# Performance work log

Measured on AMD Instinct MI355X. Metric: run time of the kernel, lower is better.

## Reference

```python
import jax, jax.numpy as jnp
import numpy as np

HIDDEN = 1024
HEADS = 16
HEAD_SIZE = HIDDEN // HEADS


def setup_inputs() -> dict:
    key = jax.random.key(0)
    k0, k1, k2, k3 = jax.random.split(key, 4)
    scale = 1.0 / np.sqrt(HIDDEN)
    return {
        "input_data": jax.random.normal(k0, (4, 4096, HIDDEN), dtype=jnp.float32),
        "W0": jax.random.normal(k1, (HIDDEN, HIDDEN), dtype=jnp.float32) * scale,
        "W1": jax.random.normal(k2, (HIDDEN, HIDDEN), dtype=jnp.float32) * scale,
        "W2": jax.random.normal(k3, (HIDDEN, HIDDEN), dtype=jnp.float32) * scale,
    }


def reference(input_data, W0, W1, W2):
    b, s, _ = input_data.shape
    k, h = HEADS, HEAD_SIZE
    # torch.nn.Linear(bias=False): y = x @ W.T
    out = input_data @ W0.T          # [b, s, hidden]
    out1 = input_data @ W1.T
    out2 = input_data @ W2.T
    # reshape to heads; cummax over the sequence axis (axis=1 here, which
    # matches cummax(dim=2) on the permuted (b,k,s,h) layout in torch)
    out_h = out.reshape(b, s, k, h)
    out1_h = out1.reshape(b, s, k, h)
    cm = jax.lax.associative_scan(jnp.maximum, (out_h + out1_h) / jnp.sqrt(jnp.float32(h)), axis=1)
    cm = cm.reshape(b, s, k * h)
    out = (cm + out2) * cm + out1
    return out
```

## Files before the change

### kernel.cpp

```cpp
#include <hip/hip_runtime.h>
#include <cstdint>
#include <cstddef>

#define HIDDEN 1024
#define BATCH 4
#define SEQ 4096
#define M_ROWS (BATCH * SEQ)
#define K_DIM 1024
#define SUBCHUNK 32
#define NSUB (SEQ / SUBCHUNK)

typedef __bf16 bf16_t;
typedef __bf16 v8bf __attribute__((ext_vector_type(8)));
typedef float v4f __attribute__((ext_vector_type(4)));
typedef unsigned short us8 __attribute__((ext_vector_type(8)));

__device__ __forceinline__ unsigned short f32_to_bf16(float f) {
  unsigned int u = __float_as_uint(f);
  u += 0x7fffu + ((u >> 16) & 1u);
  return (unsigned short)(u >> 16);
}
__device__ __forceinline__ float bf16_to_f32(unsigned short u) {
  return __uint_as_float((unsigned int)u << 16);
}

__global__ void convert_kernel(const float* __restrict__ X,
                               const float* __restrict__ W0,
                               const float* __restrict__ W1,
                               const float* __restrict__ W2,
                               unsigned short* __restrict__ Xb,
                               unsigned short* __restrict__ Wb) {
  int bx = blockIdx.x;
  if (bx < 16384) {
    int i = bx * 256 + threadIdx.x;
    float4 f = ((const float4*)X)[i];
    ushort4 u;
    u.x = f32_to_bf16(f.x); u.y = f32_to_bf16(f.y);
    u.z = f32_to_bf16(f.z); u.w = f32_to_bf16(f.w);
    ((ushort4*)Xb)[i] = u;
  } else {
    int i = (bx - 16384) * 256 + threadIdx.x;
    int mat = i >> 18;
    int off = i & 0x3FFFF;
    float4 f;
    if (mat == 0) {
      float4 a = ((const float4*)W0)[off];
      float4 b = ((const float4*)W1)[off];
      f.x = (a.x + b.x) * 0.125f; f.y = (a.y + b.y) * 0.125f;
      f.z = (a.z + b.z) * 0.125f; f.w = (a.w + b.w) * 0.125f;
    } else {
      const float* src = (mat == 1) ? W1 : W2;
      f = ((const float4*)src)[off];
    }
    ushort4 u;
    u.x = f32_to_bf16(f.x); u.y = f32_to_bf16(f.y);
    u.z = f32_to_bf16(f.z); u.w = f32_to_bf16(f.w);
    ((ushort4*)Wb)[i] = u;
  }
}

__global__ __launch_bounds__(512, 2) void gemm256_kernel(
    const bf16_t* __restrict__ A, const bf16_t* __restrict__ B,
    unsigned short* __restrict__ Lp, unsigned short* __restrict__ C1p,
    unsigned short* __restrict__ C2p, float* __restrict__ cmax) {
  extern __shared__ __align__(16) char smem[];

  const int tid = threadIdx.x;
  const int wave = tid >> 6;
  const int lane = tid & 63;
  const int quad = lane >> 4;
  const int r16 = lane & 15;
  const int wr = wave >> 2;
  const int wc = wave & 3;

  const int orig = (int)blockIdx.x;
  const int swz = (orig & 7) * 96 + (orig >> 3);
  const int bx = swz % 12;
  const int mt = swz / 12;
  const int mtile0 = mt * 256;
  const int nbase = bx * 256;

  const int l3 = lane >> 3;
  const int lc = lane & 7;
  const size_t laneOff = (size_t)l3 * K_DIM + (size_t)((lc ^ l3) << 3);
  const bf16_t* Ag = A + (size_t)(mtile0 + wave * 8) * K_DIM + laneOff;
  const bf16_t* Bg = B + (size_t)(nbase + wave * 8) * K_DIM + laneOff;

  const int aRow = (wr * 128 + r16) * 128;
  const int bRow = (wc * 64 + r16) * 128;
  const int cxor = (r16 & 7) * 16;
  const int qx = quad * 16;

  v4f acc[8][4];
#pragma unroll
  for (int i = 0; i < 8; ++i)
#pragma unroll
    for (int j = 0; j < 4; ++j) acc[i][j] = (v4f)(0.0f);

  v8bf afr[4];
  v8bf bfr[4][2];

#define STG_A(d, q, kt) __builtin_amdgcn_global_load_lds( \
    (__attribute__((address_space(1))) void*)(Ag + (size_t)(q) * (64 * K_DIM) + (size_t)(kt) * 64), \
    (__attribute__((address_space(3))) void*)(smem + (d) * 32768 + (q) * 8192 + wave * 1024), 16, 0, 0)
#define STG_B(d, q, kt) __builtin_amdgcn_global_load_lds( \
    (__attribute__((address_space(1))) void*)(Bg + (size_t)(q) * (64 * K_DIM) + (size_t)(kt) * 64), \
    (__attribute__((address_space(3))) void*)(smem + 65536 + (d) * 32768 + (q) * 8192 + wave * 1024), 16, 0, 0)
#define LDA(d, i, kk) (*(const v8bf*)(smem + (d) * 32768 + aRow + (i) * 2048 + (((kk) * 64 + qx) ^ cxor)))
#define LDB(d, j, kk) (*(const v8bf*)(smem + 65536 + (d) * 32768 + bRow + (j) * 2048 + (((kk) * 64 + qx) ^ cxor)))
#define RD_A(d, ih, kk) { _Pragma("unroll") for (int ii = 0; ii < 4; ++ii) afr[ii] = LDA(d, (ih) * 4 + ii, kk); }
#define RD_B(d, kk) { _Pragma("unroll") for (int j = 0; j < 4; ++j) bfr[j][kk] = LDB(d, j, kk); }
#define MM(ih, kk) \
  __builtin_amdgcn_s_barrier(); \
  asm volatile("s_waitcnt lgkmcnt(0)" ::: "memory"); \
  __builtin_amdgcn_s_setprio(1); \
  { _Pragma("unroll") for (int ii = 0; ii < 4; ++ii) { _Pragma("unroll") for (int j = 0; j < 4; ++j) \
      acc[(ih) * 4 + ii][j] = __builtin_amdgcn_mfma_f32_16x16x32_bf16(afr[ii], bfr[j][(kk)], acc[(ih) * 4 + ii][j], 0, 0, 0); } } \
  __builtin_amdgcn_s_setprio(0);
#define BAR() __builtin_amdgcn_s_barrier()
#define WAITV(n) asm volatile("s_waitcnt vmcnt(" #n ")" ::: "memory")

  STG_A(0, 0, 0); STG_A(0, 1, 0); STG_A(0, 2, 0); STG_A(0, 3, 0);
  STG_B(0, 0, 0); STG_B(0, 1, 0); STG_B(0, 2, 0); STG_B(0, 3, 0);
  STG_A(1, 0, 1); STG_A(1, 2, 1); STG_B(1, 0, 1); STG_B(1, 1, 1);
  WAITV(4);
  BAR();

  for (int it = 0; it < 7; ++it) {
    const int t1 = 2 * it + 1, t2 = t1 + 1, t3 = t1 + 2;
    RD_A(0, 0, 0); RD_B(0, 0);
    STG_B(1, 2, t1); STG_B(1, 3, t1);
    MM(0, 0); BAR();
    RD_B(0, 1); RD_A(0, 0, 1);
    STG_A(1, 1, t1); STG_A(1, 3, t1);
    MM(0, 1); BAR();
    RD_A(0, 1, 0);
    STG_A(0, 0, t2); STG_A(0, 2, t2);
    MM(1, 0); BAR();
    RD_A(0, 1, 1);
    STG_B(0, 0, t2); STG_B(0, 1, t2);
    MM(1, 1); WAITV(4); BAR();
    RD_A(1, 0, 0); RD_B(1, 0);
    STG_B(0, 2, t2); STG_B(0, 3, t2);
    MM(0, 0); BAR();
    RD_B(1, 1); RD_A(1, 0, 1);
    STG_A(0, 1, t2); STG_A(0, 3, t2);
    MM(0, 1); BAR();
    RD_A(1, 1, 0);
    STG_A(1, 0, t3); STG_A(1, 2, t3);
    MM(1, 0); BAR();
    RD_A(1, 1, 1);
    STG_B(1, 0, t3); STG_B(1, 1, t3);
    MM(1, 1); WAITV(4); BAR();
  }
  RD_A(0, 0, 0); RD_B(0, 0);
  STG_B(1, 2, 15); STG_B(1, 3, 15);
  MM(0, 0); BAR();
  RD_B(0, 1); RD_A(0, 0, 1);
  STG_A(1, 1, 15); STG_A(1, 3, 15);
  MM(0, 1); BAR();
  RD_A(0, 1, 0); MM(1, 0); BAR();
  RD_A(0, 1, 1); MM(1, 1); WAITV(0); BAR();
  RD_A(1, 0, 0); RD_B(1, 0); MM(0, 0); BAR();
  RD_B(1, 1); RD_A(1, 0, 1); MM(0, 1); BAR();
  RD_A(1, 1, 0); MM(1, 0); BAR();
  RD_A(1, 1, 1); MM(1, 1);

#undef STG_A
#undef STG_B
#undef LDA
#undef LDB
#undef RD_A
#undef RD_B
#undef MM
#undef BAR
#undef WAITV

  const int mat = bx >> 2;
  const int ncol0 = (bx & 3) * 256;

  if (mat != 0) {
    unsigned short* Cm = (mat == 1) ? C1p : C2p;
#pragma unroll
    for (int i = 0; i < 8; ++i)
#pragma unroll
      for (int j = 0; j < 4; ++j)
#pragma unroll
        for (int r = 0; r < 4; ++r) {
          int row = mtile0 + wr * 128 + i * 16 + quad * 4 + r;
          int col = ncol0 + wc * 64 + j * 16 + r16;
          Cm[(size_t)row * HIDDEN + col] = f32_to_bf16(acc[i][j][r]);
        }
    return;
  }

  const int bidx = mtile0 >> 12;
  const int sub0 = (mtile0 & 4095) >> 5;
#pragma unroll
  for (int s = 0; s < 4; ++s) {
#pragma unroll
    for (int j = 0; j < 4; ++j) {
      float c0[4], c1[4];
      c0[0] = acc[s * 2][j][0];
      c1[0] = acc[s * 2 + 1][j][0];
#pragma unroll
      for (int r = 1; r < 4; ++r) {
        c0[r] = fmaxf(c0[r - 1], acc[s * 2][j][r]);
        c1[r] = fmaxf(c1[r - 1], acc[s * 2 + 1][j][r]);
      }
      float t0 = c0[3], t1 = c1[3], u;
      u = __shfl_up(t0, 16); if (quad >= 1) t0 = fmaxf(t0, u);
      u = __shfl_up(t0, 32); if (quad >= 2) t0 = fmaxf(t0, u);
      u = __shfl_up(t1, 16); if (quad >= 1) t1 = fmaxf(t1, u);
      u = __shfl_up(t1, 32); if (quad >= 2) t1 = fmaxf(t1, u);
      float e0 = __shfl_up(t0, 16); if (quad == 0) e0 = -INFINITY;
      float e1 = __shfl_up(t1, 16); if (quad == 0) e1 = -INFINITY;
      float T0 = __shfl(t0, 48 + r16);
      float T1 = __shfl(t1, 48 + r16);
      int col = ncol0 + wc * 64 + j * 16 + r16;
      int rowb = mtile0 + wr * 128 + s * 32 + quad * 4;
#pragma unroll
      for (int r = 0; r < 4; ++r) {
        float L0 = fmaxf(c0[r], e0);
        float L1 = fmaxf(fmaxf(c1[r], e1), T0);
        Lp[(size_t)(rowb + r) * HIDDEN + col] = f32_to_bf16(L0);
        Lp[(size_t)(rowb + 16 + r) * HIDDEN + col] = f32_to_bf16(L1);
      }
      if (quad == 0) {
        int sub = sub0 + wr * 4 + s;
        cmax[((size_t)bidx * NSUB + sub) * HIDDEN + col] = fmaxf(T0, T1);
      }
    }
  }
}

__global__ void prefix_kernel(const float* __restrict__ cmax,
                              float* __restrict__ pmax) {
  int col = blockIdx.x * 256 + threadIdx.x;
  int b = blockIdx.y;
  const float* cp = cmax + (size_t)b * NSUB * HIDDEN + col;
  float* pp = pmax + (size_t)b * NSUB * HIDDEN + col;
  float run = -INFINITY;
#pragma unroll 1
  for (int s0 = 0; s0 < NSUB; s0 += 16) {
    float v[16];
#pragma unroll
    for (int i = 0; i < 16; ++i) v[i] = cp[(size_t)(s0 + i) * HIDDEN];
#pragma unroll
    for (int i = 0; i < 16; ++i) {
      pp[(size_t)(s0 + i) * HIDDEN] = run;
      run = fmaxf(run, v[i]);
    }
  }
}

__global__ void final_kernel(const unsigned short* __restrict__ L,
                             const unsigned short* __restrict__ C1,
                             const unsigned short* __restrict__ C2,
                             const float* __restrict__ pmax,
                             float* __restrict__ out) {
  const int t = threadIdx.x;
  const int half = t >> 7;
  const int col = (t & 127) * 8;
  const int s = blockIdx.x * 2 + half;
  const int b = blockIdx.y;
  const int sub = s >> 5;
  const float* pv = pmax + ((size_t)b * NSUB + sub) * HIDDEN + col;
  float4 p0 = *(const float4*)pv;
  float4 p1 = *(const float4*)(pv + 4);
  float pr[8] = {p0.x, p0.y, p0.z, p0.w, p1.x, p1.y, p1.z, p1.w};
  size_t base = ((size_t)b * SEQ + s) * HIDDEN + col;
  us8 ul = *(const us8*)(L + base);
  us8 u1 = *(const us8*)(C1 + base);
  us8 u2 = *(const us8*)(C2 + base);
  float o[8];
#pragma unroll
  for (int k = 0; k < 8; ++k) {
    float m = fmaxf(pr[k], bf16_to_f32((unsigned short)ul[k]));
    o[k] = (m + bf16_to_f32((unsigned short)u2[k])) * m
           + bf16_to_f32((unsigned short)u1[k]);
  }
  float4 o0 = {o[0], o[1], o[2], o[3]};
  float4 o1 = {o[4], o[5], o[6], o[7]};
  *(float4*)(out + base) = o0;
  *(float4*)(out + base + 4) = o1;
}

extern "C" void kernel_launch(void* const* d_in, const int* in_sizes, int n_in,
                              void* d_out, int out_size, void* d_ws, size_t ws_size,
                              hipStream_t stream) {
  const float* X = (const float*)d_in[0];
  const float* W0 = (const float*)d_in[1];
  const float* W1 = (const float*)d_in[2];
  const float* W2 = (const float*)d_in[3];
  float* out = (float*)d_out;

  char* ws = (char*)d_ws;
  unsigned short* Xb = (unsigned short*)ws;
  unsigned short* Wb = (unsigned short*)(ws + 33554432);
  unsigned short* Lp = (unsigned short*)(ws + 33554432 + 6291456);
  unsigned short* C1p = (unsigned short*)(ws + 2 * 33554432 + 6291456);
  unsigned short* C2p = (unsigned short*)(ws + 3 * 33554432 + 6291456);
  float* cmax = (float*)(ws + 4 * 33554432 + 6291456);
  float* pmax = (float*)(ws + 4 * 33554432 + 6291456 + 2097152);

  convert_kernel<<<19456, 256, 0, stream>>>(X, W0, W1, W2, Xb, Wb);

  gemm256_kernel<<<768, 512, 131072, stream>>>((const bf16_t*)Xb, (const bf16_t*)Wb,
                                               Lp, C1p, C2p, cmax);

  dim3 pgrid(4, BATCH);
  prefix_kernel<<<pgrid, 256, 0, stream>>>(cmax, pmax);

  dim3 fgrid(SEQ / 2, BATCH);
  final_kernel<<<fgrid, 256, 0, stream>>>(Lp, C1p, C2p, pmax, out);
}
```

Before: 158.9 us.

## Split GEMM into scan GEMM and fused W1/W2 GEMM with epilogue

The first GEMM now computes only the (W0+W1)/8 projection, producing the bf16 logits and per-chunk maxima. A second GEMM computes the W1 and W2 projections together, sharing the A tile in LDS, and applies the prefix-max combine and final formula in its epilogue, writing fp32 output directly. This drops the bf16 C1/C2 intermediate round trip through HBM and the separate elementwise final kernel. In exchange it adds a second launch that re-stages X, uses a narrower 128-column N tile per matrix, and does uncoalesced scalar Lp/pmax reads in the epilogue.

```diff
diff --git a/kernel.cpp b/kernel.cpp
--- a/kernel.cpp
+++ b/kernel.cpp
@@ -59,10 +59,9 @@
   }
 }
 
-__global__ __launch_bounds__(512, 2) void gemm256_kernel(
+__global__ __launch_bounds__(512, 2) void gemm_s_kernel(
     const bf16_t* __restrict__ A, const bf16_t* __restrict__ B,
-    unsigned short* __restrict__ Lp, unsigned short* __restrict__ C1p,
-    unsigned short* __restrict__ C2p, float* __restrict__ cmax) {
+    unsigned short* __restrict__ Lp, float* __restrict__ cmax) {
   extern __shared__ __align__(16) char smem[];
 
   const int tid = threadIdx.x;
@@ -74,9 +73,9 @@
   const int wc = wave & 3;
 
   const int orig = (int)blockIdx.x;
-  const int swz = (orig & 7) * 96 + (orig >> 3);
-  const int bx = swz % 12;
-  const int mt = swz / 12;
+  const int swz = (orig & 7) * 32 + (orig >> 3);
+  const int bx = swz & 3;
+  const int mt = swz >> 2;
   const int mtile0 = mt * 256;
   const int nbase = bx * 256;
 
@@ -176,24 +175,7 @@
 #undef BAR
 #undef WAITV
 
-  const int mat = bx >> 2;
-  const int ncol0 = (bx & 3) * 256;
-
-  if (mat != 0) {
-    unsigned short* Cm = (mat == 1) ? C1p : C2p;
-#pragma unroll
-    for (int i = 0; i < 8; ++i)
-#pragma unroll
-      for (int j = 0; j < 4; ++j)
-#pragma unroll
-        for (int r = 0; r < 4; ++r) {
-          int row = mtile0 + wr * 128 + i * 16 + quad * 4 + r;
-          int col = ncol0 + wc * 64 + j * 16 + r16;
-          Cm[(size_t)row * HIDDEN + col] = f32_to_bf16(acc[i][j][r]);
-        }
-    return;
-  }
-
+  const int ncol0 = bx * 256;
   const int bidx = mtile0 >> 12;
   const int sub0 = (mtile0 & 4095) >> 5;
 #pragma unroll
@@ -254,36 +236,149 @@
   }
 }
 
-__global__ void final_kernel(const unsigned short* __restrict__ L,
-                             const unsigned short* __restrict__ C1,
-                             const unsigned short* __restrict__ C2,
-                             const float* __restrict__ pmax,
-                             float* __restrict__ out) {
-  const int t = threadIdx.x;
-  const int half = t >> 7;
-  const int col = (t & 127) * 8;
-  const int s = blockIdx.x * 2 + half;
-  const int b = blockIdx.y;
-  const int sub = s >> 5;
-  const float* pv = pmax + ((size_t)b * NSUB + sub) * HIDDEN + col;
-  float4 p0 = *(const float4*)pv;
-  float4 p1 = *(const float4*)(pv + 4);
-  float pr[8] = {p0.x, p0.y, p0.z, p0.w, p1.x, p1.y, p1.z, p1.w};
-  size_t base = ((size_t)b * SEQ + s) * HIDDEN + col;
-  us8 ul = *(const us8*)(L + base);
-  us8 u1 = *(const us8*)(C1 + base);
-  us8 u2 = *(const us8*)(C2 + base);
-  float o[8];
-#pragma unroll
-  for (int k = 0; k < 8; ++k) {
-    float m = fmaxf(pr[k], bf16_to_f32((unsigned short)ul[k]));
-    o[k] = (m + bf16_to_f32((unsigned short)u2[k])) * m
-           + bf16_to_f32((unsigned short)u1[k]);
-  }
-  float4 o0 = {o[0], o[1], o[2], o[3]};
-  float4 o1 = {o[4], o[5], o[6], o[7]};
-  *(float4*)(out + base) = o0;
-  *(float4*)(out + base + 4) = o1;
+__global__ __launch_bounds__(512, 2) void gemm_f_kernel(
+    const bf16_t* __restrict__ A, const bf16_t* __restrict__ B,
+    const unsigned short* __restrict__ Lp, const float* __restrict__ pmax,
+    float* __restrict__ out) {
+  extern __shared__ __align__(16) char smem[];
+
+  const int tid = threadIdx.x;
+  const int wave = tid >> 6;
+  const int lane = tid & 63;
+  const int quad = lane >> 4;
+  const int r16 = lane & 15;
+  const int wr = wave >> 2;
+  const int wc = wave & 3;
+
+  const int orig = (int)blockIdx.x;
+  const int swz = (orig & 7) * 64 + (orig >> 3);
+  const int mt = swz >> 3;
+  const int nt = swz & 7;
+  const int mtile0 = mt * 256;
+  const int ncol0 = nt * 128;
+
+  const int l3 = lane >> 3;
+  const int lc = lane & 7;
+  const size_t laneOff = (size_t)l3 * K_DIM + (size_t)((lc ^ l3) << 3);
+  const bf16_t* Ag = A + (size_t)(mtile0 + wave * 8) * K_DIM + laneOff;
+  const bf16_t* Bg1 = B + (size_t)(1024 + ncol0 + wave * 8) * K_DIM + laneOff;
+  const bf16_t* Bg2 = B + (size_t)(2048 + ncol0 + wave * 8) * K_DIM + laneOff;
+
+  const int aRow = (wr * 128 + r16) * 128;
+  const int bRow = (wc * 32 + r16) * 128;
+  const int cxor = (r16 & 7) * 16;
+  const int qx = quad * 16;
+
+  v4f acc1[8][2], acc2[8][2];
+#pragma unroll
+  for (int i = 0; i < 8; ++i)
+#pragma unroll
+    for (int j = 0; j < 2; ++j) { acc1[i][j] = (v4f)(0.0f); acc2[i][j] = (v4f)(0.0f); }
+
+  v8bf afr[4];
+  v8bf b1fr[2][2], b2fr[2][2];
+
+#define STG2_A(d, q, kt) __builtin_amdgcn_global_load_lds( \
+    (__attribute__((address_space(1))) void*)(Ag + (size_t)(q) * (64 * K_DIM) + (size_t)(kt) * 64), \
+    (__attribute__((address_space(3))) void*)(smem + (d) * 32768 + (q) * 8192 + wave * 1024), 16, 0, 0)
+#define STG2_B1(d, q, kt) __builtin_amdgcn_global_load_lds( \
+    (__attribute__((address_space(1))) void*)(Bg1 + (size_t)(q) * (64 * K_DIM) + (size_t)(kt) * 64), \
+    (__attribute__((address_space(3))) void*)(smem + 65536 + (d) * 32768 + (q) * 8192 + wave * 1024), 16, 0, 0)
+#define STG2_B2(d, q, kt) __builtin_amdgcn_global_load_lds( \
+    (__attribute__((address_space(1))) void*)(Bg2 + (size_t)(q) * (64 * K_DIM) + (size_t)(kt) * 64), \
+    (__attribute__((address_space(3))) void*)(smem + 65536 + (d) * 32768 + 16384 + (q) * 8192 + wave * 1024), 16, 0, 0)
+#define LDA2(d, i, kk) (*(const v8bf*)(smem + (d) * 32768 + aRow + (i) * 2048 + (((kk) * 64 + qx) ^ cxor)))
+#define LDB21(d, j, kk) (*(const v8bf*)(smem + 65536 + (d) * 32768 + bRow + (j) * 2048 + (((kk) * 64 + qx) ^ cxor)))
+#define LDB22(d, j, kk) (*(const v8bf*)(smem + 65536 + (d) * 32768 + 16384 + bRow + (j) * 2048 + (((kk) * 64 + qx) ^ cxor)))
+#define RD2_A(d, ih, kk) { _Pragma("unroll") for (int ii = 0; ii < 4; ++ii) afr[ii] = LDA2(d, (ih) * 4 + ii, kk); }
+#define RD2_B(d, kk) { _Pragma("unroll") for (int j = 0; j < 2; ++j) { b1fr[j][kk] = LDB21(d, j, kk); b2fr[j][kk] = LDB22(d, j, kk); } }
+#define MM2(ih, kk) \
+  __builtin_amdgcn_s_barrier(); \
+  asm volatile("s_waitcnt lgkmcnt(0)" ::: "memory"); \
+  __builtin_amdgcn_s_setprio(1); \
+  { _Pragma("unroll") for (int ii = 0; ii < 4; ++ii) { _Pragma("unroll") for (int j = 0; j < 2; ++j) { \
+      acc1[(ih) * 4 + ii][j] = __builtin_amdgcn_mfma_f32_16x16x32_bf16(afr[ii], b1fr[j][(kk)], acc1[(ih) * 4 + ii][j], 0, 0, 0); \
+      acc2[(ih) * 4 + ii][j] = __builtin_amdgcn_mfma_f32_16x16x32_bf16(afr[ii], b2fr[j][(kk)], acc2[(ih) * 4 + ii][j], 0, 0, 0); } } } \
+  __builtin_amdgcn_s_setprio(0);
+#define BAR() __builtin_amdgcn_s_barrier()
+#define WAITV(n) asm volatile("s_waitcnt vmcnt(" #n ")" ::: "memory")
+
+  STG2_A(0, 0, 0); STG2_A(0, 1, 0); STG2_A(0, 2, 0); STG2_A(0, 3, 0);
+  STG2_B1(0, 0, 0); STG2_B1(0, 1, 0); STG2_B2(0, 0, 0); STG2_B2(0, 1, 0);
+  STG2_A(1, 0, 1); STG2_A(1, 2, 1); STG2_B1(1, 0, 1); STG2_B1(1, 1, 1);
+  WAITV(4);
+  BAR();
+
+  for (int it = 0; it < 7; ++it) {
+    const int t1 = 2 * it + 1, t2 = t1 + 1, t3 = t1 + 2;
+    RD2_A(0, 0, 0); RD2_B(0, 0);
+    STG2_B2(1, 0, t1); STG2_B2(1, 1, t1);
+    MM2(0, 0); BAR();
+    RD2_B(0, 1); RD2_A(0, 0, 1);
+    STG2_A(1, 1, t1); STG2_A(1, 3, t1);
+    MM2(0, 1); BAR();
+    RD2_A(0, 1, 0);
+    STG2_A(0, 0, t2); STG2_A(0, 2, t2);
+    MM2(1, 0); BAR();
+    RD2_A(0, 1, 1);
+    STG2_B1(0, 0, t2); STG2_B1(0, 1, t2);
+    MM2(1, 1); WAITV(4); BAR();
+    RD2_A(1, 0, 0); RD2_B(1, 0);
+    STG2_B2(0, 0, t2); STG2_B2(0, 1, t2);
+    MM2(0, 0); BAR();
+    RD2_B(1, 1); RD2_A(1, 0, 1);
+    STG2_A(0, 1, t2); STG2_A(0, 3, t2);
+    MM2(0, 1); BAR();
+    RD2_A(1, 1, 0);
+    STG2_A(1, 0, t3); STG2_A(1, 2, t3);
+    MM2(1, 0); BAR();
+    RD2_A(1, 1, 1);
+    STG2_B1(1, 0, t3); STG2_B1(1, 1, t3);
+    MM2(1, 1); WAITV(4); BAR();
+  }
+  RD2_A(0, 0, 0); RD2_B(0, 0);
+  STG2_B2(1, 0, 15); STG2_B2(1, 1, 15);
+  MM2(0, 0); BAR();
+  RD2_B(0, 1); RD2_A(0, 0, 1);
+  STG2_A(1, 1, 15); STG2_A(1, 3, 15);
+  MM2(0, 1); BAR();
+  RD2_A(0, 1, 0); MM2(1, 0); BAR();
+  RD2_A(0, 1, 1); MM2(1, 1); WAITV(0); BAR();
+  RD2_A(1, 0, 0); RD2_B(1, 0); MM2(0, 0); BAR();
+  RD2_B(1, 1); RD2_A(1, 0, 1); MM2(0, 1); BAR();
+  RD2_A(1, 1, 0); MM2(1, 0); BAR();
+  RD2_A(1, 1, 1); MM2(1, 1);
+
+#undef STG2_A
+#undef STG2_B1
+#undef STG2_B2
+#undef LDA2
+#undef LDB21
+#undef LDB22
+#undef RD2_A
+#undef RD2_B
+#undef MM2
+#undef BAR
+#undef WAITV
+
+  const int bidx = mtile0 >> 12;
+  const int sub0 = (mtile0 & 4095) >> 5;
+#pragma unroll
+  for (int i = 0; i < 8; ++i) {
+    const int subr = sub0 + wr * 4 + (i >> 1);
+#pragma unroll
+    for (int j = 0; j < 2; ++j) {
+      const int col = ncol0 + wc * 32 + j * 16 + r16;
+      const float pm = pmax[((size_t)bidx * NSUB + subr) * HIDDEN + col];
+      const int row0 = mtile0 + wr * 128 + i * 16 + quad * 4;
+#pragma unroll
+      for (int r = 0; r < 4; ++r) {
+        size_t idx = (size_t)(row0 + r) * HIDDEN + col;
+        float m = fmaxf(pm, bf16_to_f32(Lp[idx]));
+        out[idx] = (m + acc2[i][j][r]) * m + acc1[i][j][r];
+      }
+    }
+  }
 }
 
 extern "C" void kernel_launch(void* const* d_in, const int* in_sizes, int n_in,
@@ -299,19 +394,17 @@
   unsigned short* Xb = (unsigned short*)ws;
   unsigned short* Wb = (unsigned short*)(ws + 33554432);
   unsigned short* Lp = (unsigned short*)(ws + 33554432 + 6291456);
-  unsigned short* C1p = (unsigned short*)(ws + 2 * 33554432 + 6291456);
-  unsigned short* C2p = (unsigned short*)(ws + 3 * 33554432 + 6291456);
   float* cmax = (float*)(ws + 4 * 33554432 + 6291456);
   float* pmax = (float*)(ws + 4 * 33554432 + 6291456 + 2097152);
 
   convert_kernel<<<19456, 256, 0, stream>>>(X, W0, W1, W2, Xb, Wb);
 
-  gemm256_kernel<<<768, 512, 131072, stream>>>((const bf16_t*)Xb, (const bf16_t*)Wb,
-                                               Lp, C1p, C2p, cmax);
+  gemm_s_kernel<<<256, 512, 131072, stream>>>((const bf16_t*)Xb, (const bf16_t*)Wb,
+                                              Lp, cmax);
 
   dim3 pgrid(4, BATCH);
   prefix_kernel<<<pgrid, 256, 0, stream>>>(cmax, pmax);
 
-  dim3 fgrid(SEQ / 2, BATCH);
-  final_kernel<<<fgrid, 256, 0, stream>>>(Lp, C1p, C2p, pmax, out);
-}
+  gemm_f_kernel<<<512, 512, 131072, stream>>>((const bf16_t*)Xb, (const bf16_t*)Wb,
+                                              Lp, pmax, out);
+}
```

Result: faster. 131.1 us (-17.5%).
